# Kernel tuning notes

Hardware: AMD Instinct MI355X
Metric: run time of the kernel (lower is better)

The kernel has to match this reference:

```python
import jax, jax.numpy as jnp
import numpy as np

BUCKET_SIZE = 64
N_HASHES = 8
SELF_ATTN_MASK_VAL = -10000.0


def look_one_back(x):
    # concat each chunk with the previous chunk along the within-chunk axis (axis=2)
    prev = jnp.concatenate([x[:, -1:], x[:, :-1]], axis=1)
    return jnp.concatenate([x, prev], axis=2)


def setup_inputs() -> dict:
    key = jax.random.key(0)
    b, s, d = 4, 4096, 64
    n_buckets = s // BUCKET_SIZE  # 64
    kq, kk, kv, kr = jax.random.split(key, 4)
    return {
        "q": jax.random.normal(kq, (b, s, d), jnp.float32),
        "k": jax.random.normal(kk, (b, s, d), jnp.float32),
        "v": jax.random.normal(kv, (b, s, d), jnp.float32),
        "rotations": jax.random.normal(kr, (d, N_HASHES, n_buckets // 2), jnp.float32),
    }


def reference(q, k, v, rotations):
    b, s, d = q.shape
    n_buckets = s // BUCKET_SIZE
    n_chunks = N_HASHES * n_buckets

    # ---- hash_vectors: random-rotation LSH bucketing on q ----
    rot = jnp.einsum('bsd,dhn->bhsn', q, rotations)           # [b, nh, s, nb/2]
    rot = jnp.concatenate([rot, -rot], axis=-1)               # [b, nh, s, nb]
    buckets = jnp.argmax(rot, axis=-1)                        # [b, nh, s]
    offsets = (jnp.arange(N_HASHES) * n_buckets)[None, :, None]
    buckets = (buckets + offsets).reshape(b, N_HASHES * s)    # [b, nh*s]

    # ---- sort tokens by (bucket, position) ----
    ticker = jnp.broadcast_to(jnp.arange(N_HASHES * s), (b, N_HASHES * s))
    buckets_and_t = s * buckets + (ticker % s)
    sticker = jnp.argsort(buckets_and_t, axis=-1)             # sort permutation
    sbuckets_and_t = jnp.take_along_axis(buckets_and_t, sticker, axis=-1)
    undo_sort = jnp.argsort(sticker, axis=-1)
    st = sticker % s                                          # original positions

    gather_seq = lambda x, idx: jnp.take_along_axis(x, idx[..., None], axis=1)
    sq = gather_seq(q, st)
    sk = gather_seq(k, st)
    sv = gather_seq(v, st)

    bq_t = st.reshape(b, n_chunks, -1)                        # [b, n, s_c]
    bq = sq.reshape(b, n_chunks, -1, d)
    bk = sk.reshape(b, n_chunks, -1, d)
    bv = sv.reshape(b, n_chunks, -1, d)

    bk = bk / jnp.linalg.norm(bk, axis=-1, keepdims=True)
    bk = look_one_back(bk)                                    # [b, n, 2*s_c, d]
    bv = look_one_back(bv)
    bkv_t = look_one_back(bq_t)                               # [b, n, 2*s_c]

    dots = jnp.einsum('bnsd,bnzd->bnsz', bq, bk) * (d ** -0.5)
    masked_value = -jnp.finfo(dots.dtype).max

    # self-attention mask (soft, matches torch SELF_ATTN_MASK_VAL)
    self_mask = bq_t[:, :, :, None] == bkv_t[:, :, None, :]
    dots = jnp.where(self_mask, SELF_ATTN_MASK_VAL, dots)

    # do not attend across buckets
    bq_buckets = (sbuckets_and_t // s).reshape(b, n_chunks, -1)
    bkv_buckets = look_one_back(bq_buckets)
    bucket_mask = bq_buckets[:, :, :, None] != bkv_buckets[:, :, None, :]
    dots = jnp.where(bucket_mask, masked_value, dots)

    # duplicate-attention correction
    locs1 = undo_sort // BUCKET_SIZE
    locs2 = (locs1 + 1) % n_chunks
    locs1 = buckets * n_chunks + locs1
    locs2 = buckets * n_chunks + locs2
    locs = jnp.concatenate([locs1.reshape(b, N_HASHES, s),
                            locs2.reshape(b, N_HASHES, s)], axis=1)
    locs = jnp.transpose(locs, (0, 2, 1))                     # [b, s, 2*nh]
    slocs = jnp.take_along_axis(locs, st[..., None], axis=1)  # [b, nh*s, 2*nh]
    b_locs = slocs.reshape(b, n_chunks, -1, 2 * N_HASHES)
    bq_locs = jnp.concatenate([b_locs[..., :N_HASHES], b_locs[..., :N_HASHES]], axis=-1)
    bkv_locs = look_one_back(b_locs)                          # [b, n, 2*s_c, 2*nh]
    dup_counts = jnp.sum(bq_locs[:, :, :, None, :] == bkv_locs[:, :, None, :, :], axis=-1)
    dots = dots - jnp.log(dup_counts.astype(dots.dtype) + 1e-9)

    # softmax (stable) and attention output
    dots_lse = jax.nn.logsumexp(dots, axis=-1, keepdims=True)
    probs_chunk = jnp.exp(dots - dots_lse)
    bo = jnp.einsum('bnsz,bnzd->bnsd', probs_chunk, bv)

    # unsort and combine across hash rounds
    so = bo.reshape(b, -1, d)
    o = jnp.take_along_axis(so, undo_sort[..., None], axis=1).reshape(b, N_HASHES, s, d)
    slogits = dots_lse.reshape(b, -1)
    logits = jnp.take_along_axis(slogits, undo_sort, axis=1).reshape(b, N_HASHES, s, 1)
    probs = jnp.exp(logits - jax.nn.logsumexp(logits, axis=1, keepdims=True))
    out = jnp.sum(o * probs, axis=1)                          # [b, s, d]
    return out
```

## Files before the change

kernel.cpp:

```cpp
#include <hip/hip_runtime.h>
#include <hip/hip_bf16.h>
#include <math.h>

constexpr int B   = 4;
constexpr int S   = 4096;
constexpr int D   = 64;
constexpr int NH  = 8;
constexpr int NB  = 64;
constexpr int NBT = 512;
constexpr int NI  = NH * S;
constexpr int NCH = 512;
constexpr int CHB = 256;

typedef __attribute__((ext_vector_type(8))) _Float16 f16x8;
typedef __attribute__((ext_vector_type(2))) __fp16 fp16x2;
typedef __attribute__((ext_vector_type(4))) float f32x4;
typedef __attribute__((ext_vector_type(2))) unsigned short u16x2;

constexpr float LOG2E = 1.44269504088896341f;

__device__ __forceinline__ unsigned short f16b(float x) {
    _Float16 h = (_Float16)x;
    return __builtin_bit_cast(unsigned short, h);
}
__device__ __forceinline__ unsigned pk_rne(float a, float b) {
    return (unsigned)f16b(a) | ((unsigned)f16b(b) << 16);
}
__device__ __forceinline__ u16x2 nm2(int a, int b) {
    u16x2 x = __builtin_bit_cast(u16x2, a ^ b);
    u16x2 one = {1, 1};
    return __builtin_elementwise_min(x, one);
}
__device__ __forceinline__ unsigned pk16(float a, float b) {
    fp16x2 hp = __builtin_amdgcn_cvt_pkrtz(a, b);
    return __builtin_bit_cast(unsigned, hp);
}
template <int CTRL>
__device__ __forceinline__ float dppf(float x) {
    return __builtin_bit_cast(float,
        __builtin_amdgcn_update_dpp(__builtin_bit_cast(int, x), __builtin_bit_cast(int, x),
                                    CTRL, 0xF, 0xF, false));
}

__global__ __launch_bounds__(256)
void k_hash(const float* __restrict__ q, const float* __restrict__ k,
            const float* __restrict__ v, const float* __restrict__ rot,
            int* __restrict__ buckets, int* __restrict__ counts, int* __restrict__ tot,
            unsigned short* __restrict__ q16, unsigned short* __restrict__ kn16,
            unsigned short* __restrict__ v16) {
    int blk = blockIdx.x;
    int tko = blk & 31, h = (blk >> 5) & 7, b = blk >> 8;
    __shared__ __align__(16) float rs[64 * 36];
    __shared__ int hist[64];
    int tid = threadIdx.x;
    if (tid < 64) hist[tid] = 0;
    for (int i = tid; i < 2048; i += 256) {
        int nn = i & 31, d = i >> 5;
        rs[d * 36 + nn] = rot[(d * 8 + h) * 32 + nn];
    }
    __syncthreads();
    int ng = tid & 7, tg = tid >> 3;
    int t0 = tko * 128 + tg * 4;
    const float* qp = q + ((size_t)b * S + t0) * 64;
    float acc[4][4] = {};
    #pragma unroll 4
    for (int d4 = 0; d4 < 16; ++d4) {
        f32x4 r4[4];
        #pragma unroll
        for (int dd = 0; dd < 4; ++dd)
            r4[dd] = *(const f32x4*)(rs + (4 * d4 + dd) * 36 + 4 * ng);
        #pragma unroll
        for (int i = 0; i < 4; ++i) {
            f32x4 q4 = *(const f32x4*)(qp + i * 64 + d4 * 4);
            #pragma unroll
            for (int dd = 0; dd < 4; ++dd)
                #pragma unroll
                for (int c = 0; c < 4; ++c)
                    acc[i][c] += q4[dd] * r4[dd][c];
        }
    }
    #pragma unroll
    for (int i = 0; i < 4; ++i) {
        float vp = -3.402823466e38f, vn = -3.402823466e38f;
        int ip = 0, in_ = 0;
        #pragma unroll
        for (int c = 0; c < 4; ++c) {
            float a = acc[i][c]; int idx = 4 * ng + c;
            if (a > vp)  { vp = a;  ip = idx; }
            if (-a > vn) { vn = -a; in_ = idx; }
        }
        #pragma unroll
        for (int off = 1; off < 8; off <<= 1) {
            float ov = __shfl_xor(vp, off); int oi = __shfl_xor(ip, off);
            if (ov > vp || (ov == vp && oi < ip)) { vp = ov; ip = oi; }
            ov = __shfl_xor(vn, off); oi = __shfl_xor(in_, off);
            if (ov > vn || (ov == vn && oi < in_)) { vn = ov; in_ = oi; }
        }
        if (ng == 0) {
            int bi = (vn > vp) ? (in_ + 32) : ip;
            buckets[b * NI + h * 4096 + t0 + i] = bi + h * NB;
            atomicAdd(&hist[bi], 1);
        }
    }
    __syncthreads();
    if (tid < 64) {
        int cnt = hist[tid];
        counts[((size_t)b * NBT + h * 64 + tid) * 32 + tko] = cnt;
        atomicAdd(&tot[b * NBT + h * 64 + tid], cnt);
    }

    if (h == 0) {
        int r  = tko * 128 + (tid >> 1);
        int hf = tid & 1;
        size_t base = ((size_t)b * S + r) * 64 + hf * 32;
        f32x4 rv[8];
        float ss = 0.f;
        #pragma unroll
        for (int j = 0; j < 8; ++j) {
            rv[j] = *(const f32x4*)(k + base + 4 * j);
            ss += rv[j][0]*rv[j][0] + rv[j][1]*rv[j][1] + rv[j][2]*rv[j][2] + rv[j][3]*rv[j][3];
        }
        ss += __shfl_xor(ss, 1);
        float sc = rsqrtf(ss);
        unsigned ow[16];
        #pragma unroll
        for (int i = 0; i < 16; ++i) {
            float a  = rv[i >> 1][(i & 1) * 2] * sc;
            float bb = rv[i >> 1][(i & 1) * 2 + 1] * sc;
            ow[i] = pk_rne(a, bb);
        }
        *(uint4*)(kn16 + base)      = make_uint4(ow[0], ow[1], ow[2], ow[3]);
        *(uint4*)(kn16 + base + 8)  = make_uint4(ow[4], ow[5], ow[6], ow[7]);
        *(uint4*)(kn16 + base + 16) = make_uint4(ow[8], ow[9], ow[10], ow[11]);
        *(uint4*)(kn16 + base + 24) = make_uint4(ow[12], ow[13], ow[14], ow[15]);
        const float qsc = 0.125f * LOG2E;
        #pragma unroll
        for (int j = 0; j < 8; ++j) rv[j] = *(const f32x4*)(q + base + 4 * j);
        #pragma unroll
        for (int i = 0; i < 16; ++i)
            ow[i] = pk_rne(rv[i >> 1][(i & 1) * 2] * qsc, rv[i >> 1][(i & 1) * 2 + 1] * qsc);
        *(uint4*)(q16 + base)      = make_uint4(ow[0], ow[1], ow[2], ow[3]);
        *(uint4*)(q16 + base + 8)  = make_uint4(ow[4], ow[5], ow[6], ow[7]);
        *(uint4*)(q16 + base + 16) = make_uint4(ow[8], ow[9], ow[10], ow[11]);
        *(uint4*)(q16 + base + 24) = make_uint4(ow[12], ow[13], ow[14], ow[15]);
        #pragma unroll
        for (int j = 0; j < 8; ++j) rv[j] = *(const f32x4*)(v + base + 4 * j);
        #pragma unroll
        for (int i = 0; i < 16; ++i)
            ow[i] = pk_rne(rv[i >> 1][(i & 1) * 2], rv[i >> 1][(i & 1) * 2 + 1]);
        *(uint4*)(v16 + base)      = make_uint4(ow[0], ow[1], ow[2], ow[3]);
        *(uint4*)(v16 + base + 8)  = make_uint4(ow[4], ow[5], ow[6], ow[7]);
        *(uint4*)(v16 + base + 16) = make_uint4(ow[8], ow[9], ow[10], ow[11]);
        *(uint4*)(v16 + base + 24) = make_uint4(ow[12], ow[13], ow[14], ow[15]);
    }
}

__global__ void k_scatter(const int* __restrict__ buckets, const int* __restrict__ counts,
                          const int* __restrict__ tot, int* __restrict__ spos,
                          int* __restrict__ undo, unsigned short* __restrict__ locU) {
    int b = blockIdx.x >> 8, c = blockIdx.x & 255;
    int h = c >> 5, tko = c & 31;
    __shared__ int bk_s[128];
    __shared__ int sbase[NBT];
    __shared__ int pfx[64];
    __shared__ int wsum[2];
    int tid = threadIdx.x;
    int lane = tid & 63, w = tid >> 6;
    int4 tv = *(const int4*)(tot + b * NBT + tid * 4);
    int part = tv.x + tv.y + tv.z + tv.w;
    int incl = part;
    #pragma unroll
    for (int off = 1; off < 64; off <<= 1) {
        int t_ = __shfl_up(incl, off);
        if (lane >= off) incl += t_;
    }
    if (lane == 63) wsum[w] = incl;
    int bl = tid >> 1, hf = tid & 1;
    const int* crow = counts + ((size_t)b * NBT + h * 64 + bl) * 32 + hf * 16;
    int ps = 0;
    #pragma unroll
    for (int jj = 0; jj < 4; ++jj) {
        int4 cv = *(const int4*)(crow + jj * 4);
        int bi = hf * 16 + jj * 4;
        ps += (bi + 0 < tko) ? cv.x : 0;
        ps += (bi + 1 < tko) ? cv.y : 0;
        ps += (bi + 2 < tko) ? cv.z : 0;
        ps += (bi + 3 < tko) ? cv.w : 0;
    }
    ps += __shfl_xor(ps, 1);
    int i_flat = c * 128 + tid;
    int bkt = buckets[b * NI + i_flat];
    bk_s[tid] = bkt;
    if (hf == 0) pfx[bl] = ps;
    __syncthreads();
    if (w == 1) incl += wsum[0];
    int excl = incl - part;
    sbase[4 * tid]     = excl;
    sbase[4 * tid + 1] = excl + tv.x;
    sbase[4 * tid + 2] = excl + tv.x + tv.y;
    sbase[4 * tid + 3] = excl + tv.x + tv.y + tv.z;
    __syncthreads();
    int rank = 0;
    for (int j = 0; j < 128; ++j) {
        int vv = bk_s[j];
        rank += (j < tid && vv == bkt);
    }
    int pos = sbase[bkt] + pfx[bkt - h * 64] + rank;
    spos[b * NI + pos] = (i_flat & 4095) | (bkt << 12);
    undo[b * NI + i_flat] = pos;
    int t = i_flat & 4095;
    locU[(((size_t)b << 12) | t) * 8 + h] =
        (unsigned short)(((bkt & 63) << 9) | (pos >> 6));
}

__device__ __forceinline__ int bump_loc(int k1) {
    return (k1 & 0x7E007E00) | ((k1 + 0x00010001) & 0x01FF01FF);
}

__global__ __launch_bounds__(256, 2)
void k_attn(const unsigned short* __restrict__ q16, const unsigned short* __restrict__ kn16,
            const unsigned short* __restrict__ v16, const int* __restrict__ spos,
            const int4* __restrict__ loc1P, unsigned short* __restrict__ soh,
            float* __restrict__ slog) {
    int n = blockIdx.x & 511, b = blockIdx.x >> 9;
    __shared__ __align__(16) char buf[31488];
    unsigned short* qs = (unsigned short*)buf;
    unsigned short* ks = (unsigned short*)(buf + 9216);
    unsigned short* ph = (unsigned short*)buf;
    unsigned short* vh = (unsigned short*)(buf + 9216);
    int* klocs1 = (int*)(buf + 27648);
    int* qlocs  = (int*)(buf + 29696);
    int* mq     = (int*)(buf + 30720);
    int* mk     = (int*)(buf + 30976);

    int tid = threadIdx.x;
    int bni = b * NI;
    const unsigned short* q16b = q16 + ((size_t)b << 12) * 64;
    const unsigned short* kn16b = kn16 + ((size_t)b << 12) * 64;
    const unsigned short* v16b = v16 + ((size_t)b << 12) * 64;

    if (tid < 64) mq[tid] = spos[bni + n * 64 + tid];
    else if (tid < 192) {
        int z = tid - 64;
        int nn = (z < 64) ? n : ((n + 511) & 511);
        mk[z] = spos[bni + nn * 64 + (z & 63)];
    }
    __syncthreads();

    #pragma unroll
    for (int it = 0; it < 2; ++it) {
        int i = it * 256 + tid;
        int row = i >> 3, c8 = i & 7;
        int t = mq[row] & 4095;
        uint4 val = *(const uint4*)(q16b + (size_t)t * 64 + c8 * 8);
        *(uint4*)(qs + row * 72 + c8 * 8) = val;
    }
    #pragma unroll
    for (int it = 0; it < 4; ++it) {
        int i = it * 256 + tid;
        int row = i >> 3, c8 = i & 7;
        int t = mk[row] & 4095;
        uint4 val = *(const uint4*)(kn16b + (size_t)t * 64 + c8 * 8);
        *(uint4*)(ks + row * 72 + c8 * 8) = val;
    }
    if (tid < 128) {
        int t = mk[tid] & 4095;
        *(int4*)(klocs1 + tid * 4) = loc1P[((size_t)b << 12) | t];
    } else if (tid < 192) {
        int r = tid - 128;
        int tq = mq[r] & 4095;
        *(int4*)(qlocs + r * 4) = loc1P[((size_t)b << 12) | tq];
    }
    __syncthreads();

    int li = tid & 15, hi4 = (tid >> 4) & 3, w = tid >> 6;

    f32x4 sacc[8];
    {
        f16x8 a0 = *(f16x8*)(qs + (16 * w + li) * 72 + 8 * hi4);
        f16x8 a1 = *(f16x8*)(qs + (16 * w + li) * 72 + 32 + 8 * hi4);
        #pragma unroll
        for (int zt = 0; zt < 8; ++zt) {
            f16x8 b0 = *(f16x8*)(ks + (16 * zt + li) * 72 + 8 * hi4);
            f16x8 b1 = *(f16x8*)(ks + (16 * zt + li) * 72 + 32 + 8 * hi4);
            f32x4 c = {0.f, 0.f, 0.f, 0.f};
            c = __builtin_amdgcn_mfma_f32_16x16x32_f16(a0, b0, c, 0, 0, 0);
            c = __builtin_amdgcn_mfma_f32_16x16x32_f16(a1, b1, c, 0, 0, 0);
            sacc[zt] = c;
        }
    }

    int tqr[4], bqr[4];
    int4 lq[4];
    #pragma unroll
    for (int j = 0; j < 4; ++j) {
        int R = 16 * w + 4 * hi4 + j;
        int m = mq[R];
        tqr[j] = m & 4095; bqr[j] = m >> 12;
        lq[j] = *(const int4*)(qlocs + R * 4);
    }
    #pragma unroll
    for (int zt = 0; zt < 8; ++zt) {
        int z = 16 * zt + li;
        int mz = mk[z]; int tk = mz & 4095, bk = mz >> 12;
        int4 k1 = *(const int4*)(klocs1 + z * 4);
        int4 k2;
        k2.x = bump_loc(k1.x); k2.y = bump_loc(k1.y);
        k2.z = bump_loc(k1.z); k2.w = bump_loc(k1.w);
        #pragma unroll
        for (int j = 0; j < 4; ++j) {
            float s = sacc[zt][j];
            if (tqr[j] == tk) s = -14426.950408f;
            if (bqr[j] != bk) s = -3.402823466e38f;
            u16x2 acc = nm2(lq[j].x, k1.x);
            acc = acc + nm2(lq[j].y, k1.y);
            acc = acc + nm2(lq[j].z, k1.z);
            acc = acc + nm2(lq[j].w, k1.w);
            acc = acc + nm2(lq[j].x, k2.x);
            acc = acc + nm2(lq[j].y, k2.y);
            acc = acc + nm2(lq[j].z, k2.z);
            acc = acc + nm2(lq[j].w, k2.w);
            unsigned ua = __builtin_bit_cast(unsigned, acc);
            int dup = 16 - (int)((ua & 0xffffu) + (ua >> 16));
            s -= log2f(fmaxf((float)dup, 1.0f));
            sacc[zt][j] = s;
        }
    }

    float inv[4];
    #pragma unroll
    for (int j = 0; j < 4; ++j) {
        float m = sacc[0][j];
        #pragma unroll
        for (int zt = 1; zt < 8; ++zt) m = fmaxf(m, sacc[zt][j]);
        m = fmaxf(m, dppf<0x121>(m));
        m = fmaxf(m, dppf<0x122>(m));
        m = fmaxf(m, dppf<0x124>(m));
        m = fmaxf(m, dppf<0x128>(m));
        float sum = 0.f;
        #pragma unroll
        for (int zt = 0; zt < 8; ++zt) {
            float e = exp2f(sacc[zt][j] - m);
            sacc[zt][j] = e; sum += e;
        }
        sum += dppf<0x121>(sum);
        sum += dppf<0x122>(sum);
        sum += dppf<0x124>(sum);
        sum += dppf<0x128>(sum);
        float lse = m + log2f(sum);
        inv[j] = __builtin_amdgcn_rcpf(sum);
        if (li == 0) slog[bni + n * 64 + 16 * w + 4 * hi4 + j] = lse;
    }
    __syncthreads();

    #pragma unroll
    for (int it = 0; it < 8; ++it) {
        int i = it * 256 + tid;
        int zp = i & 63;
        int dp = i >> 6;
        int t0 = mk[2 * zp] & 4095, t1 = mk[2 * zp + 1] & 4095;
        unsigned a = *(const unsigned*)(v16b + (size_t)t0 * 64 + 2 * dp);
        unsigned c = *(const unsigned*)(v16b + (size_t)t1 * 64 + 2 * dp);
        *(unsigned*)(vh + (2 * dp) * 136 + 2 * zp)     = __builtin_amdgcn_perm(c, a, 0x05040100u);
        *(unsigned*)(vh + (2 * dp + 1) * 136 + 2 * zp) = __builtin_amdgcn_perm(c, a, 0x07060302u);
    }
    f32x4 oacc[4] = {{0,0,0,0},{0,0,0,0},{0,0,0,0},{0,0,0,0}};
    #pragma unroll
    for (int half = 0; half < 2; ++half) {
        #pragma unroll
        for (int zt4 = 0; zt4 < 4; ++zt4) {
            int zt = half * 4 + zt4;
            #pragma unroll
            for (int j = 0; j < 4; ++j) {
                float p  = sacc[zt][j] * inv[j];
                float po = dppf<0xB1>(p);
                if ((li & 1) == 0) {
                    int R  = 16 * w + 4 * hi4 + j;
                    int zl = 16 * zt4 + li;
                    *(unsigned*)(ph + R * 72 + zl) = pk16(p, po);
                }
            }
        }
        __syncthreads();
        #pragma unroll
        for (int step = 0; step < 2; ++step) {
            f16x8 pa = *(f16x8*)(ph + (16 * w + li) * 72 + 32 * step + 8 * hi4);
            #pragma unroll
            for (int nt = 0; nt < 4; ++nt) {
                f16x8 vb = *(f16x8*)(vh + (16 * nt + li) * 136 + 64 * half + 32 * step + 8 * hi4);
                oacc[nt] = __builtin_amdgcn_mfma_f32_16x16x32_f16(pa, vb, oacc[nt], 0, 0, 0);
            }
        }
        __syncthreads();
    }

    size_t ob = ((size_t)bni + n * 64) * 64;
    #pragma unroll
    for (int nt = 0; nt < 4; ++nt)
        #pragma unroll
        for (int j = 0; j < 4; ++j) {
            float o  = oacc[nt][j];
            float oo = dppf<0xB1>(o);
            if ((li & 1) == 0) {
                *(unsigned*)(soh + ob + (size_t)(16 * w + 4 * hi4 + j) * 64 + 16 * nt + li) =
                    pk16(o, oo);
            }
        }
}

__global__ void k_comb(const int* __restrict__ undo, const float* __restrict__ slog,
                       const unsigned short* __restrict__ soh, float* __restrict__ out) {
    int flatT = blockIdx.x * 4 + (threadIdx.x >> 6);
    int lane  = threadIdx.x & 63;
    int b = flatT >> 12, t = flatT & (S - 1);
    int ph[NH]; float lg[NH];
    float m = -3.402823466e38f;
#pragma unroll
    for (int h = 0; h < NH; ++h) {
        ph[h] = undo[b * NI + (h << 12) + t];
        lg[h] = slog[b * NI + ph[h]];
        m = fmaxf(m, lg[h]);
    }
    float sum = 0.f;
#pragma unroll
    for (int h = 0; h < NH; ++h) sum += exp2f(lg[h] - m);
    float lse2 = m + log2f(sum);
    float o = 0.f;
#pragma unroll
    for (int h = 0; h < NH; ++h) {
        float wgt = exp2f(lg[h] - lse2);
        _Float16 hv = *(const _Float16*)(soh + ((size_t)b * NI + ph[h]) * D + lane);
        o += wgt * (float)hv;
    }
    out[(size_t)flatT * D + lane] = o;
}

extern "C" void kernel_launch(void* const* d_in, const int* in_sizes, int n_in,
                              void* d_out, int out_size, void* d_ws, size_t ws_size,
                              hipStream_t stream) {
    const float* q   = (const float*)d_in[0];
    const float* k   = (const float*)d_in[1];
    const float* v   = (const float*)d_in[2];
    const float* rot = (const float*)d_in[3];
    float* out = (float*)d_out;

    char* ws = (char*)d_ws;
    size_t off = 0;
    auto alloc = [&](size_t bytes) -> void* {
        void* p = ws + off;
        off += (bytes + 255) & ~(size_t)255;
        return p;
    };
    unsigned short* q16  = (unsigned short*)alloc((size_t)B * S * D * 2);
    unsigned short* kn16 = (unsigned short*)alloc((size_t)B * S * D * 2);
    unsigned short* v16  = (unsigned short*)alloc((size_t)B * S * D * 2);
    unsigned short* soh  = (unsigned short*)alloc((size_t)B * NI * D * 2);
    float* slog    = (float*)alloc((size_t)B * NI * 4);
    int*   buckets = (int*)alloc((size_t)B * NI * 4);
    int*   counts  = (int*)alloc((size_t)B * NBT * 32 * 4);
    int*   tot     = (int*)alloc((size_t)B * NBT * 4);
    int*   spos    = (int*)alloc((size_t)B * NI * 4);
    int*   undo    = (int*)alloc((size_t)B * NI * 4);
    unsigned short* locU = (unsigned short*)alloc((size_t)B * S * NH * 2);

    hipMemsetAsync(tot, 0, (size_t)B * NBT * 4, stream);
    k_hash<<<1024, 256, 0, stream>>>(q, k, v, rot, buckets, counts, tot, q16, kn16, v16);
    k_scatter<<<B * CHB, 128, 0, stream>>>(buckets, counts, tot, spos, undo, locU);
    k_attn<<<B * NCH, 256, 0, stream>>>(q16, kn16, v16, spos, (const int4*)locU, soh, slog);
    k_comb<<<B * S / 4, 256, 0, stream>>>(undo, slog, soh, out);
}
```

Baseline: 110.7 us.

## Split fp16 conversion into own kernel and restructure attention kernel loads

The q/k/v fp16 conversion and k-normalisation move out of the hash kernel (where only h==0 blocks did them) into a separate prep kernel with one wavefront per row. In the attention kernel, Q fragments are loaded straight from global memory into registers instead of staged through LDS. V gathers are issued into registers before the softmax so their latency overlaps with computation, and P gets its own LDS region, which removes two barriers in the PV loop. The cost is an extra kernel launch, higher register pressure in the attention kernel, and scalar 2-byte stores in the prep kernel.

```diff
diff --git a/kernel.cpp b/kernel.cpp
--- a/kernel.cpp
+++ b/kernel.cpp
@@ -23,9 +23,6 @@
     _Float16 h = (_Float16)x;
     return __builtin_bit_cast(unsigned short, h);
 }
-__device__ __forceinline__ unsigned pk_rne(float a, float b) {
-    return (unsigned)f16b(a) | ((unsigned)f16b(b) << 16);
-}
 __device__ __forceinline__ u16x2 nm2(int a, int b) {
     u16x2 x = __builtin_bit_cast(u16x2, a ^ b);
     u16x2 one = {1, 1};
@@ -42,12 +39,24 @@
                                     CTRL, 0xF, 0xF, false));
 }
 
+__global__ void k_prep(const float* __restrict__ q, const float* __restrict__ k,
+                       const float* __restrict__ v, unsigned short* __restrict__ q16,
+                       unsigned short* __restrict__ kn16, unsigned short* __restrict__ v16) {
+    int row  = blockIdx.x * 4 + (threadIdx.x >> 6);
+    int lane = threadIdx.x & 63;
+    size_t idx = (size_t)row * 64 + lane;
+    float kv = k[idx];
+    float ss = kv * kv;
+#pragma unroll
+    for (int m = 1; m < 64; m <<= 1) ss += __shfl_xor(ss, m, 64);
+    kn16[idx] = f16b(kv / sqrtf(ss));
+    q16[idx]  = f16b(q[idx] * (0.125f * LOG2E));
+    v16[idx]  = f16b(v[idx]);
+}
+
 __global__ __launch_bounds__(256)
-void k_hash(const float* __restrict__ q, const float* __restrict__ k,
-            const float* __restrict__ v, const float* __restrict__ rot,
-            int* __restrict__ buckets, int* __restrict__ counts, int* __restrict__ tot,
-            unsigned short* __restrict__ q16, unsigned short* __restrict__ kn16,
-            unsigned short* __restrict__ v16) {
+void k_hash(const float* __restrict__ q, const float* __restrict__ rot,
+            int* __restrict__ buckets, int* __restrict__ counts, int* __restrict__ tot) {
     int blk = blockIdx.x;
     int tko = blk & 31, h = (blk >> 5) & 7, b = blk >> 8;
     __shared__ __align__(16) float rs[64 * 36];
@@ -107,51 +116,6 @@
         int cnt = hist[tid];
         counts[((size_t)b * NBT + h * 64 + tid) * 32 + tko] = cnt;
         atomicAdd(&tot[b * NBT + h * 64 + tid], cnt);
-    }
-
-    if (h == 0) {
-        int r  = tko * 128 + (tid >> 1);
-        int hf = tid & 1;
-        size_t base = ((size_t)b * S + r) * 64 + hf * 32;
-        f32x4 rv[8];
-        float ss = 0.f;
-        #pragma unroll
-        for (int j = 0; j < 8; ++j) {
-            rv[j] = *(const f32x4*)(k + base + 4 * j);
-            ss += rv[j][0]*rv[j][0] + rv[j][1]*rv[j][1] + rv[j][2]*rv[j][2] + rv[j][3]*rv[j][3];
-        }
-        ss += __shfl_xor(ss, 1);
-        float sc = rsqrtf(ss);
-        unsigned ow[16];
-        #pragma unroll
-        for (int i = 0; i < 16; ++i) {
-            float a  = rv[i >> 1][(i & 1) * 2] * sc;
-            float bb = rv[i >> 1][(i & 1) * 2 + 1] * sc;
-            ow[i] = pk_rne(a, bb);
-        }
-        *(uint4*)(kn16 + base)      = make_uint4(ow[0], ow[1], ow[2], ow[3]);
-        *(uint4*)(kn16 + base + 8)  = make_uint4(ow[4], ow[5], ow[6], ow[7]);
-        *(uint4*)(kn16 + base + 16) = make_uint4(ow[8], ow[9], ow[10], ow[11]);
-        *(uint4*)(kn16 + base + 24) = make_uint4(ow[12], ow[13], ow[14], ow[15]);
-        const float qsc = 0.125f * LOG2E;
-        #pragma unroll
-        for (int j = 0; j < 8; ++j) rv[j] = *(const f32x4*)(q + base + 4 * j);
-        #pragma unroll
-        for (int i = 0; i < 16; ++i)
-            ow[i] = pk_rne(rv[i >> 1][(i & 1) * 2] * qsc, rv[i >> 1][(i & 1) * 2 + 1] * qsc);
-        *(uint4*)(q16 + base)      = make_uint4(ow[0], ow[1], ow[2], ow[3]);
-        *(uint4*)(q16 + base + 8)  = make_uint4(ow[4], ow[5], ow[6], ow[7]);
-        *(uint4*)(q16 + base + 16) = make_uint4(ow[8], ow[9], ow[10], ow[11]);
-        *(uint4*)(q16 + base + 24) = make_uint4(ow[12], ow[13], ow[14], ow[15]);
-        #pragma unroll
-        for (int j = 0; j < 8; ++j) rv[j] = *(const f32x4*)(v + base + 4 * j);
-        #pragma unroll
-        for (int i = 0; i < 16; ++i)
-            ow[i] = pk_rne(rv[i >> 1][(i & 1) * 2], rv[i >> 1][(i & 1) * 2 + 1]);
-        *(uint4*)(v16 + base)      = make_uint4(ow[0], ow[1], ow[2], ow[3]);
-        *(uint4*)(v16 + base + 8)  = make_uint4(ow[4], ow[5], ow[6], ow[7]);
-        *(uint4*)(v16 + base + 16) = make_uint4(ow[8], ow[9], ow[10], ow[11]);
-        *(uint4*)(v16 + base + 24) = make_uint4(ow[12], ow[13], ow[14], ow[15]);
     }
 }
 
@@ -224,10 +188,9 @@
             float* __restrict__ slog) {
     int n = blockIdx.x & 511, b = blockIdx.x >> 9;
     __shared__ __align__(16) char buf[31488];
-    unsigned short* qs = (unsigned short*)buf;
-    unsigned short* ks = (unsigned short*)(buf + 9216);
-    unsigned short* ph = (unsigned short*)buf;
-    unsigned short* vh = (unsigned short*)(buf + 9216);
+    unsigned short* ks = (unsigned short*)buf;
+    unsigned short* vh = (unsigned short*)buf;
+    unsigned short* ph = (unsigned short*)(buf + 18432);
     int* klocs1 = (int*)(buf + 27648);
     int* qlocs  = (int*)(buf + 29696);
     int* mq     = (int*)(buf + 30720);
@@ -247,14 +210,8 @@
     }
     __syncthreads();
 
-    #pragma unroll
-    for (int it = 0; it < 2; ++it) {
-        int i = it * 256 + tid;
-        int row = i >> 3, c8 = i & 7;
-        int t = mq[row] & 4095;
-        uint4 val = *(const uint4*)(q16b + (size_t)t * 64 + c8 * 8);
-        *(uint4*)(qs + row * 72 + c8 * 8) = val;
-    }
+    int li = tid & 15, hi4 = (tid >> 4) & 3, w = tid >> 6;
+
     #pragma unroll
     for (int it = 0; it < 4; ++it) {
         int i = it * 256 + tid;
@@ -271,23 +228,31 @@
         int tq = mq[r] & 4095;
         *(int4*)(qlocs + r * 4) = loc1P[((size_t)b << 12) | tq];
     }
-    __syncthreads();
-
-    int li = tid & 15, hi4 = (tid >> 4) & 3, w = tid >> 6;
+    int myqrow = mq[16 * w + li] & 4095;
+    f16x8 a0 = *(const f16x8*)(q16b + (size_t)myqrow * 64 + 8 * hi4);
+    f16x8 a1 = *(const f16x8*)(q16b + (size_t)myqrow * 64 + 32 + 8 * hi4);
+    __syncthreads();
 
     f32x4 sacc[8];
-    {
-        f16x8 a0 = *(f16x8*)(qs + (16 * w + li) * 72 + 8 * hi4);
-        f16x8 a1 = *(f16x8*)(qs + (16 * w + li) * 72 + 32 + 8 * hi4);
-        #pragma unroll
-        for (int zt = 0; zt < 8; ++zt) {
-            f16x8 b0 = *(f16x8*)(ks + (16 * zt + li) * 72 + 8 * hi4);
-            f16x8 b1 = *(f16x8*)(ks + (16 * zt + li) * 72 + 32 + 8 * hi4);
-            f32x4 c = {0.f, 0.f, 0.f, 0.f};
-            c = __builtin_amdgcn_mfma_f32_16x16x32_f16(a0, b0, c, 0, 0, 0);
-            c = __builtin_amdgcn_mfma_f32_16x16x32_f16(a1, b1, c, 0, 0, 0);
-            sacc[zt] = c;
-        }
+    #pragma unroll
+    for (int zt = 0; zt < 8; ++zt) {
+        f16x8 b0 = *(f16x8*)(ks + (16 * zt + li) * 72 + 8 * hi4);
+        f16x8 b1 = *(f16x8*)(ks + (16 * zt + li) * 72 + 32 + 8 * hi4);
+        f32x4 c = {0.f, 0.f, 0.f, 0.f};
+        c = __builtin_amdgcn_mfma_f32_16x16x32_f16(a0, b0, c, 0, 0, 0);
+        c = __builtin_amdgcn_mfma_f32_16x16x32_f16(a1, b1, c, 0, 0, 0);
+        sacc[zt] = c;
+    }
+
+    unsigned vfa[8], vfb[8];
+    #pragma unroll
+    for (int it = 0; it < 8; ++it) {
+        int i = it * 256 + tid;
+        int zp = i & 63;
+        int dp = i >> 6;
+        int t0 = mk[2 * zp] & 4095, t1 = mk[2 * zp + 1] & 4095;
+        vfa[it] = *(const unsigned*)(v16b + (size_t)t0 * 64 + 2 * dp);
+        vfb[it] = *(const unsigned*)(v16b + (size_t)t1 * 64 + 2 * dp);
     }
 
     int tqr[4], bqr[4];
@@ -356,14 +321,13 @@
     #pragma unroll
     for (int it = 0; it < 8; ++it) {
         int i = it * 256 + tid;
-        int zp = i & 63;
-        int dp = i >> 6;
-        int t0 = mk[2 * zp] & 4095, t1 = mk[2 * zp + 1] & 4095;
-        unsigned a = *(const unsigned*)(v16b + (size_t)t0 * 64 + 2 * dp);
-        unsigned c = *(const unsigned*)(v16b + (size_t)t1 * 64 + 2 * dp);
+        int zp = i & 63, dp = i >> 6;
+        unsigned a = vfa[it], c = vfb[it];
         *(unsigned*)(vh + (2 * dp) * 136 + 2 * zp)     = __builtin_amdgcn_perm(c, a, 0x05040100u);
         *(unsigned*)(vh + (2 * dp + 1) * 136 + 2 * zp) = __builtin_amdgcn_perm(c, a, 0x07060302u);
     }
+    __syncthreads();
+
     f32x4 oacc[4] = {{0,0,0,0},{0,0,0,0},{0,0,0,0},{0,0,0,0}};
     #pragma unroll
     for (int half = 0; half < 2; ++half) {
@@ -381,7 +345,6 @@
                 }
             }
         }
-        __syncthreads();
         #pragma unroll
         for (int step = 0; step < 2; ++step) {
             f16x8 pa = *(f16x8*)(ph + (16 * w + li) * 72 + 32 * step + 8 * hi4);
@@ -391,7 +354,6 @@
                 oacc[nt] = __builtin_amdgcn_mfma_f32_16x16x32_f16(pa, vb, oacc[nt], 0, 0, 0);
             }
         }
-        __syncthreads();
     }
 
     size_t ob = ((size_t)bni + n * 64) * 64;
@@ -464,7 +426,8 @@
     unsigned short* locU = (unsigned short*)alloc((size_t)B * S * NH * 2);
 
     hipMemsetAsync(tot, 0, (size_t)B * NBT * 4, stream);
-    k_hash<<<1024, 256, 0, stream>>>(q, k, v, rot, buckets, counts, tot, q16, kn16, v16);
+    k_prep<<<B * S / 4, 256, 0, stream>>>(q, k, v, q16, kn16, v16);
+    k_hash<<<1024, 256, 0, stream>>>(q, rot, buckets, counts, tot);
     k_scatter<<<B * CHB, 128, 0, stream>>>(buckets, counts, tot, spos, undo, locU);
     k_attn<<<B * NCH, 256, 0, stream>>>(q16, kn16, v16, spos, (const int4*)locU, soh, slog);
     k_comb<<<B * S / 4, 256, 0, stream>>>(undo, slog, soh, out);
```

Result: faster. 102.3 us (-7.7%).
